# Performance work log

Hardware: AMD Instinct MI355X
Metric: run time of the kernel (lower is better)

The kernel has to match this reference:

```python
import jax, jax.numpy as jnp
import numpy as np

# ---- ANI symmetry-function constants (from __init__ defaults) ----
N_ATOMS = 50000
N_ELEMENTS = 7
RADIAL_CUTOFF = 5.1      # angstrom
ANGULAR_CUTOFF = 3.5     # angstrom
RADIAL_START = 0.8
ANGULAR_START = 0.8
RADIAL_DIV = 8           # radial_sublength = 8
ANGULAR_DIV = 8
ANGLE_SECTIONS = 4       # angular sublength = 4*8 = 32
ETA_R = 19.7
ETA_A = 12.5
ZETA = 14.1

ShfR = np.linspace(RADIAL_START, RADIAL_CUTOFF, RADIAL_DIV + 1, dtype=np.float32)[:-1]
ShfA = np.linspace(ANGULAR_START, ANGULAR_CUTOFF, ANGULAR_DIV + 1, dtype=np.float32)[:-1]
ShfZ = ((np.arange(ANGLE_SECTIONS, dtype=np.float32) + 0.5) * np.pi / ANGLE_SECTIONS)


def cosine_cutoff(d, rc):
    return jnp.where(d <= rc, 0.5 * jnp.cos(jnp.pi * d / rc) + 0.5, 0.0)


def setup_inputs() -> dict:
    key = jax.random.key(0)
    k1, k2, k3, k4, k5 = jax.random.split(key, 5)
    n_pairs, n_trip = 1_600_000, 1_600_000
    # pair distances in [0.8, 5.1)
    r_ij = jax.random.uniform(k1, (n_pairs,), jnp.float32) * (RADIAL_CUTOFF - RADIAL_START) + RADIAL_START
    pair_indices = jax.random.randint(k2, (2, n_pairs), 0, N_ATOMS, jnp.int32)
    atomic_numbers = jax.random.randint(k3, (N_ATOMS,), 0, N_ELEMENTS, jnp.int32)
    # triplet displacement vectors with norms in [0.8, 3.5)
    dirs = jax.random.normal(k4, (2, n_trip, 3), jnp.float32)
    dirs = dirs / jnp.linalg.norm(dirs, axis=-1, keepdims=True)
    mags = jax.random.uniform(k5, (2, n_trip, 1), jnp.float32) * (ANGULAR_CUTOFF - ANGULAR_START) + ANGULAR_START
    vec12 = dirs * mags
    return {"r_ij": r_ij, "pair_indices": pair_indices,
            "atomic_numbers": atomic_numbers, "vec12": vec12}


def _radial_features(d):
    # [P, 8]: ANI radial symmetry function
    fc = cosine_cutoff(d, RADIAL_CUTOFF)
    g = 0.25 * jnp.exp(-ETA_R * (d[:, None] - jnp.asarray(ShfR)) ** 2)
    return g * fc[:, None]


def _angular_features(vec12):
    v1, v2 = vec12[0], vec12[1]                       # [T, 3]
    d1 = jnp.linalg.norm(v1, axis=-1)
    d2 = jnp.linalg.norm(v2, axis=-1)
    cos_t = 0.95 * jnp.sum(v1 * v2, axis=-1) / (d1 * d2)
    theta = jnp.arccos(cos_t)                         # [T]
    f_ang = ((1.0 + jnp.cos(theta[:, None] - jnp.asarray(ShfZ))) * 0.5) ** ZETA   # [T, 4]
    f_rad = jnp.exp(-ETA_A * (0.5 * (d1 + d2)[:, None] - jnp.asarray(ShfA)) ** 2) # [T, 8]
    fc = cosine_cutoff(d1, ANGULAR_CUTOFF) * cosine_cutoff(d2, ANGULAR_CUTOFF)    # [T]
    ang = 2.0 * f_ang[:, :, None] * f_rad[:, None, :] * fc[:, None, None]          # [T, 4, 8]
    return ang.reshape(ang.shape[0], ANGLE_SECTIONS * ANGULAR_DIV)                 # [T, 32]


def reference(r_ij, pair_indices, atomic_numbers, vec12):
    # radial branch
    feat = _radial_features(r_ij)                     # [P, 8]
    species12 = atomic_numbers[pair_indices]          # [2, P]
    index12 = pair_indices * N_ELEMENTS + species12[::-1]  # flip(0): use partner species
    aev = jnp.zeros((N_ATOMS * N_ELEMENTS, RADIAL_DIV), feat.dtype)
    aev = aev.at[index12[0]].add(feat).at[index12[1]].add(feat)
    # angular branch
    ang = _angular_features(vec12)                    # [T, 32]
    return (aev, ang)
```

## Files before the change

### kernel.cpp

```cpp
#include <hip/hip_runtime.h>


#define N_ATOMS 50000
#define N_ELEM 7
#define RADIAL_DIV 8
#define NROWS (N_ATOMS * N_ELEM)

constexpr float RADIAL_CUTOFF = 5.1f;
constexpr float ANGULAR_CUTOFF = 3.5f;
constexpr float ETA_R = 19.7f;
constexpr float ETA_A = 12.5f;
constexpr float ZETA = 14.1f;
constexpr float PI_F = 3.14159265358979323846f;
constexpr float FP_SCALE = 4096.0f;
constexpr float FP_INV = 1.0f / 4096.0f;
constexpr float SHELL_STEP = 0.5375f;
constexpr float INV_SHELL_STEP = 1.0f / 0.5375f;

__device__ __constant__ float CSZ[4] = { 0.9238795325f,  0.3826834324f, -0.3826834324f, -0.9238795325f };
__device__ __constant__ float SNZ[4] = { 0.3826834324f,  0.9238795325f,  0.9238795325f,  0.3826834324f };

#define BLK 256

__global__ __launch_bounds__(BLK) void fused_kernel(
        const float* __restrict__ r_ij,
        const int* __restrict__ pair_idx,
        const int* __restrict__ Z,
        unsigned long long* __restrict__ acc,
        int P,
        const float* __restrict__ vec12,
        float* __restrict__ ang,
        int T,
        int nRad, int nAng) {
    __shared__ float sm[BLK * 33];
    int bid = blockIdx.x;
    int tid = threadIdx.x;

    int paired = min(nRad, nAng);
    bool isAng;
    int id;
    if (bid < 2 * paired) {
        isAng = ((bid & 1) == 0);
        id = bid >> 1;
    } else {
        id = bid - paired;
        isAng = (nAng > nRad);
    }

    if (!isAng) {
        int t = id * BLK + tid;
        if (t >= P) return;
        float d = r_ij[t];
        float fc = (d <= RADIAL_CUTOFF)
                       ? (0.5f * __cosf(PI_F * d * (1.0f / RADIAL_CUTOFF)) + 0.5f)
                       : 0.0f;

        float x = (d - 0.8f) * INV_SHELL_STEP;
        int k0 = (int)(x + 0.5f);
        k0 = min(max(k0, 1), 6);
        int a = k0 - 1;
        int g = a >> 1;
        int sh = (a & 1) << 4;

        unsigned long long w = 0ull;
        #pragma unroll
        for (int j = 0; j < 3; j++) {
            float diff = d - (0.8f + SHELL_STEP * (float)(a + j));
            float gv = 0.25f * __expf(-ETA_R * diff * diff) * fc;
            unsigned int q = (unsigned int)(gv * FP_SCALE + 0.5f);
            w |= (unsigned long long)q << (16 * j);
        }
        w <<= sh;
        if (w == 0ull) return;

        int i0 = pair_idx[t];
        int i1 = pair_idx[P + t];
        int s0 = Z[i0];
        int s1 = Z[i1];
        atomicAdd(acc + ((size_t)i0 * N_ELEM + s1) * 3 + g, w);
        atomicAdd(acc + ((size_t)i1 * N_ELEM + s0) * 3 + g, w);
        return;
    }

    int t = id * BLK + tid;
    float vals[32];
    if (t < T) {
        const float* v1 = vec12 + 3ull * (size_t)t;
        const float* v2 = vec12 + 3ull * (size_t)T + 3ull * (size_t)t;
        float x1 = v1[0], y1 = v1[1], z1 = v1[2];
        float x2 = v2[0], y2 = v2[1], z2 = v2[2];

        float d1 = sqrtf(x1 * x1 + y1 * y1 + z1 * z1);
        float d2 = sqrtf(x2 * x2 + y2 * y2 + z2 * z2);
        float dot = x1 * x2 + y1 * y2 + z1 * z2;
        float cost = 0.95f * dot / (d1 * d2);
        float sint = sqrtf(fmaxf(0.0f, 1.0f - cost * cost));

        float fc1 = (d1 <= ANGULAR_CUTOFF) ? (0.5f * __cosf(PI_F * d1 * (1.0f / ANGULAR_CUTOFF)) + 0.5f) : 0.0f;
        float fc2 = (d2 <= ANGULAR_CUTOFF) ? (0.5f * __cosf(PI_F * d2 * (1.0f / ANGULAR_CUTOFF)) + 0.5f) : 0.0f;
        float fc = fc1 * fc2;

        float davg = 0.5f * (d1 + d2);
        float frad[8];
        #pragma unroll
        for (int k = 0; k < 8; k++) {
            float diff = davg - (0.8f + 0.3375f * (float)k);
            frad[k] = __expf(-ETA_A * diff * diff);
        }
        #pragma unroll
        for (int j = 0; j < 4; j++) {
            float c = 0.5f * (1.0f + cost * CSZ[j] + sint * SNZ[j]);
            float base = 2.0f * __powf(c, ZETA) * fc;
            #pragma unroll
            for (int k = 0; k < 8; k++) vals[j * 8 + k] = base * frad[k];
        }
    } else {
        #pragma unroll
        for (int k = 0; k < 32; k++) vals[k] = 0.0f;
    }

    #pragma unroll
    for (int k = 0; k < 32; k++) sm[tid * 33 + k] = vals[k];
    __syncthreads();

    size_t base = (size_t)id * BLK * 32;
    size_t lim = (size_t)T * 32;
    #pragma unroll
    for (int it = 0; it < 8; it++) {
        int f = it * BLK + tid;
        int row = f >> 3;
        int col = (f & 7) * 4;
        float4 o;
        o.x = sm[row * 33 + col + 0];
        o.y = sm[row * 33 + col + 1];
        o.z = sm[row * 33 + col + 2];
        o.w = sm[row * 33 + col + 3];
        size_t gidx = base + (size_t)f * 4;
        if (gidx < lim) reinterpret_cast<float4*>(ang)[gidx >> 2] = o;
    }
}

__global__ void convert_kernel(const unsigned long long* __restrict__ acc,
                               float* __restrict__ aev, int nrows) {
    int r = blockIdx.x * blockDim.x + threadIdx.x;
    if (r >= nrows) return;
    unsigned long long g0 = acc[3 * (size_t)r + 0];
    unsigned long long g1 = acc[3 * (size_t)r + 1];
    unsigned long long g2 = acc[3 * (size_t)r + 2];
    unsigned int l0[4], l1[4], l2[4];
    #pragma unroll
    for (int j = 0; j < 4; j++) {
        l0[j] = (unsigned int)(g0 >> (16 * j)) & 0xFFFFu;
        l1[j] = (unsigned int)(g1 >> (16 * j)) & 0xFFFFu;
        l2[j] = (unsigned int)(g2 >> (16 * j)) & 0xFFFFu;
    }
    float4 oa, ob;
    oa.x = (float)(l0[0])         * FP_INV;
    oa.y = (float)(l0[1])         * FP_INV;
    oa.z = (float)(l0[2] + l1[0]) * FP_INV;
    oa.w = (float)(l0[3] + l1[1]) * FP_INV;
    ob.x = (float)(l1[2] + l2[0]) * FP_INV;
    ob.y = (float)(l1[3] + l2[1]) * FP_INV;
    ob.z = (float)(l2[2])         * FP_INV;
    ob.w = (float)(l2[3])         * FP_INV;
    float4* o = reinterpret_cast<float4*>(aev + 8ull * (size_t)r);
    o[0] = oa;
    o[1] = ob;
}

extern "C" void kernel_launch(void* const* d_in, const int* in_sizes, int n_in,
                              void* d_out, int out_size, void* d_ws, size_t ws_size,
                              hipStream_t stream) {
    const float* r_ij     = (const float*)d_in[0];
    const int*   pair_idx = (const int*)d_in[1];
    const int*   Z        = (const int*)d_in[2];
    const float* vec12    = (const float*)d_in[3];

    const int P = in_sizes[0];
    const int T = in_sizes[3] / 6;

    float* aev = (float*)d_out;
    float* ang = aev + (size_t)NROWS * RADIAL_DIV;

    unsigned long long* acc = (unsigned long long*)d_ws;
    hipMemsetAsync(acc, 0, (size_t)NROWS * 3 * sizeof(unsigned long long), stream);

    const int nRad = (P + BLK - 1) / BLK;
    const int nAng = (T + BLK - 1) / BLK;
    fused_kernel<<<dim3(nRad + nAng), dim3(BLK), 0, stream>>>(
        r_ij, pair_idx, Z, acc, P, vec12, ang, T, nRad, nAng);
    convert_kernel<<<dim3((NROWS + 255) / 256), dim3(256), 0, stream>>>(acc, aev, NROWS);
}
```

Measured before the change: 369.7 us.

## Replicate radial accumulators to spread atomics and interleave blocks in groups of eight

Radial-branch atomics now go to up to 8 replicated copies of the fixed-point accumulator, chosen by block index, and the convert kernel sums the replicas. The aim is to cut atomic contention and same-address serialization. Block interleaving between angular and radial work changes from alternating single blocks to alternating groups of 8. The cost is a larger memset, extra workspace traffic in convert, and reduced L2 locality for atomics. Packed 16-bit lanes may now overflow only if sums exceed the limit, and since replicas sum in 32-bit this should be safe.

Result: slower. 429.2 us (+16.1%).

```diff
diff --git a/kernel.cpp b/kernel.cpp
--- a/kernel.cpp
+++ b/kernel.cpp
@@ -31,20 +31,24 @@
         const float* __restrict__ vec12,
         float* __restrict__ ang,
         int T,
-        int nRad, int nAng) {
+        int nRad, int nAng, int repMask) {
     __shared__ float sm[BLK * 33];
     int bid = blockIdx.x;
     int tid = threadIdx.x;
 
-    int paired = min(nRad, nAng);
+    int fullG = (min(nRad, nAng)) >> 3;
+    int base = fullG * 16;
     bool isAng;
     int id;
-    if (bid < 2 * paired) {
-        isAng = ((bid & 1) == 0);
-        id = bid >> 1;
+    if (bid < base) {
+        int grp = bid >> 3;
+        isAng = ((grp & 1) == 0);
+        id = (grp >> 1) * 8 + (bid & 7);
     } else {
-        id = bid - paired;
-        isAng = (nAng > nRad);
+        int l = bid - base;
+        int angLeft = nAng - fullG * 8;
+        if (l < angLeft) { isAng = true;  id = fullG * 8 + l; }
+        else             { isAng = false; id = fullG * 8 + (l - angLeft); }
     }
 
     if (!isAng) {
@@ -73,12 +77,14 @@
         w <<= sh;
         if (w == 0ull) return;
 
+        unsigned long long* accr = acc + (size_t)(bid & repMask) * NROWS * 3;
+
         int i0 = pair_idx[t];
         int i1 = pair_idx[P + t];
         int s0 = Z[i0];
         int s1 = Z[i1];
-        atomicAdd(acc + ((size_t)i0 * N_ELEM + s1) * 3 + g, w);
-        atomicAdd(acc + ((size_t)i1 * N_ELEM + s0) * 3 + g, w);
+        atomicAdd(accr + ((size_t)i0 * N_ELEM + s1) * 3 + g, w);
+        atomicAdd(accr + ((size_t)i1 * N_ELEM + s0) * 3 + g, w);
         return;
     }
 
@@ -110,9 +116,9 @@
         #pragma unroll
         for (int j = 0; j < 4; j++) {
             float c = 0.5f * (1.0f + cost * CSZ[j] + sint * SNZ[j]);
-            float base = 2.0f * __powf(c, ZETA) * fc;
+            float base2 = 2.0f * __powf(c, ZETA) * fc;
             #pragma unroll
-            for (int k = 0; k < 8; k++) vals[j * 8 + k] = base * frad[k];
+            for (int k = 0; k < 8; k++) vals[j * 8 + k] = base2 * frad[k];
         }
     } else {
         #pragma unroll
@@ -123,7 +129,7 @@
     for (int k = 0; k < 32; k++) sm[tid * 33 + k] = vals[k];
     __syncthreads();
 
-    size_t base = (size_t)id * BLK * 32;
+    size_t obase = (size_t)id * BLK * 32;
     size_t lim = (size_t)T * 32;
     #pragma unroll
     for (int it = 0; it < 8; it++) {
@@ -135,24 +141,29 @@
         o.y = sm[row * 33 + col + 1];
         o.z = sm[row * 33 + col + 2];
         o.w = sm[row * 33 + col + 3];
-        size_t gidx = base + (size_t)f * 4;
+        size_t gidx = obase + (size_t)f * 4;
         if (gidx < lim) reinterpret_cast<float4*>(ang)[gidx >> 2] = o;
     }
 }
 
 __global__ void convert_kernel(const unsigned long long* __restrict__ acc,
-                               float* __restrict__ aev, int nrows) {
+                               float* __restrict__ aev, int nrows, int R) {
     int r = blockIdx.x * blockDim.x + threadIdx.x;
     if (r >= nrows) return;
-    unsigned long long g0 = acc[3 * (size_t)r + 0];
-    unsigned long long g1 = acc[3 * (size_t)r + 1];
-    unsigned long long g2 = acc[3 * (size_t)r + 2];
-    unsigned int l0[4], l1[4], l2[4];
-    #pragma unroll
-    for (int j = 0; j < 4; j++) {
-        l0[j] = (unsigned int)(g0 >> (16 * j)) & 0xFFFFu;
-        l1[j] = (unsigned int)(g1 >> (16 * j)) & 0xFFFFu;
-        l2[j] = (unsigned int)(g2 >> (16 * j)) & 0xFFFFu;
+    unsigned int l0[4] = {0, 0, 0, 0};
+    unsigned int l1[4] = {0, 0, 0, 0};
+    unsigned int l2[4] = {0, 0, 0, 0};
+    for (int rep = 0; rep < R; rep++) {
+        const unsigned long long* a = acc + (size_t)rep * nrows * 3 + 3 * (size_t)r;
+        unsigned long long g0 = a[0];
+        unsigned long long g1 = a[1];
+        unsigned long long g2 = a[2];
+        #pragma unroll
+        for (int j = 0; j < 4; j++) {
+            l0[j] += (unsigned int)(g0 >> (16 * j)) & 0xFFFFu;
+            l1[j] += (unsigned int)(g1 >> (16 * j)) & 0xFFFFu;
+            l2[j] += (unsigned int)(g2 >> (16 * j)) & 0xFFFFu;
+        }
     }
     float4 oa, ob;
     oa.x = (float)(l0[0])         * FP_INV;
@@ -182,12 +193,16 @@
     float* aev = (float*)d_out;
     float* ang = aev + (size_t)NROWS * RADIAL_DIV;
 
+    const size_t repBytes = (size_t)NROWS * 3 * sizeof(unsigned long long);
+    int R = 1;
+    while (R < 8 && (size_t)(2 * R) * repBytes <= ws_size) R <<= 1;
+
     unsigned long long* acc = (unsigned long long*)d_ws;
-    hipMemsetAsync(acc, 0, (size_t)NROWS * 3 * sizeof(unsigned long long), stream);
+    hipMemsetAsync(acc, 0, (size_t)R * repBytes, stream);
 
     const int nRad = (P + BLK - 1) / BLK;
     const int nAng = (T + BLK - 1) / BLK;
     fused_kernel<<<dim3(nRad + nAng), dim3(BLK), 0, stream>>>(
-        r_ij, pair_idx, Z, acc, P, vec12, ang, T, nRad, nAng);
-    convert_kernel<<<dim3((NROWS + 255) / 256), dim3(256), 0, stream>>>(acc, aev, NROWS);
+        r_ij, pair_idx, Z, acc, P, vec12, ang, T, nRad, nAng, R - 1);
+    convert_kernel<<<dim3((NROWS + 255) / 256), dim3(256), 0, stream>>>(acc, aev, NROWS, R);
 }
```
